# Kernel optimization log

Measured on AMD Instinct MI355X. Metric: run time of the kernel, lower is better.

## Reference

```python
import jax, jax.numpy as jnp
import numpy as np

WS = 8        # window_size
OWIN = 12     # overlap_win_size = int(8*0.5)+8
PAD = 2       # (OWIN - WS)//2
HEADS = 4
DH = 16
INNER = HEADS * DH  # 64
DIM = 64


def _unfold(x, ws=WS, owin=OWIN, pad=PAD):
    # torch nn.Unfold(kernel=(owin,owin), stride=ws, padding=pad):
    # output [b, C*owin*owin, L] with channel ordering (c, kh, kw), L row-major over windows
    b, c, h, w = x.shape
    xp = jnp.pad(x, ((0, 0), (0, 0), (pad, pad), (pad, pad)))
    nH, nW = h // ws, w // ws
    ri = (jnp.arange(nH) * ws)[:, None] + jnp.arange(owin)[None, :]  # [nH, owin]
    ci = (jnp.arange(nW) * ws)[:, None] + jnp.arange(owin)[None, :]  # [nW, owin]
    p = xp[:, :, ri, :]          # [b, c, nH, owin, Wp]
    p = p[:, :, :, :, ci]        # [b, c, nH, owin, nW, owin]
    p = p.transpose(0, 1, 3, 5, 2, 4)  # [b, c, kh, kw, nH, nW]
    return p.reshape(b, c * owin * owin, nH * nW)


def setup_inputs() -> dict:
    key = jax.random.key(0)
    k1, k2, k3 = jax.random.split(key, 3)
    x = jax.random.normal(k1, (1, DIM, 64, 64), jnp.float32)
    w_qkv = jax.random.normal(k2, (3 * INNER, DIM), jnp.float32) * 0.05  # 1x1 conv, no bias
    w_out = jax.random.normal(k3, (DIM, INNER), jnp.float32) * 0.05     # 1x1 conv, no bias
    ln_w = jnp.ones((DIM,), jnp.float32)
    return {"x": x, "w_qkv": w_qkv, "w_out": w_out, "ln_w": ln_w}


def reference(x, w_qkv, w_out, ln_w):
    b, c, h, w = x.shape
    # BiasFree LayerNorm over channel dim (no mean subtraction)
    xc = x.transpose(0, 2, 3, 1)                       # b h w c
    var = jnp.var(xc, axis=-1, keepdims=True)
    xn = (xc / jnp.sqrt(var + 1e-5) * ln_w).transpose(0, 3, 1, 2)
    # qkv 1x1 conv
    qkv = jnp.einsum('bchw,oc->bohw', xn, w_qkv)
    qs, ks, vs = jnp.split(qkv, 3, axis=1)
    # queries: all h*w positions
    qs = qs.transpose(0, 2, 3, 1).reshape(b, h * w, HEADS, DH).transpose(0, 2, 1, 3)  # b heads N dh
    # keys/values: overlapping unfolded windows (faithful to torch reshape order)
    kk = _unfold(ks).reshape(b, INNER, -1).reshape(b, HEADS, -1, DH)  # b heads M dh
    vv = _unfold(vs).reshape(b, INNER, -1).reshape(b, HEADS, -1, DH)
    # rel_pos and fixed_mask are all-zero tensors in the source -> no-op bias
    attn = jnp.einsum('bhnd,bhmd->bhnm', qs, kk) * (DH ** -0.5)
    attn = jax.nn.softmax(attn, axis=-1)
    out = jnp.einsum('bhnm,bhmd->bhnd', attn, vv)
    out = out.transpose(0, 2, 1, 3).reshape(b, h, w, INNER).transpose(0, 3, 1, 2)
    return jnp.einsum('bchw,oc->bohw', out, w_out)
```

## Files before the change

### kernel.cpp

```cpp
#include <hip/hip_runtime.h>
#include <math.h>

#define PIX 4096
typedef unsigned short ushort_t;
typedef unsigned int uint_t;
typedef __attribute__((ext_vector_type(8))) short bf16x8;
typedef __attribute__((ext_vector_type(16))) float f32x16;

#define OFF_APART 524288
#define OFF_USHORT 2752512
#define U_QH 0
#define U_KF 262144
#define U_VF 851968

#define QSCALE 0.36067376022224087f

#if defined(__has_builtin)
#if __has_builtin(__builtin_amdgcn_exp2f)
#define EXP2F(x) __builtin_amdgcn_exp2f(x)
#endif
#if __has_builtin(__builtin_amdgcn_perm)
#define PKHI16(u1, u0) __builtin_amdgcn_perm((u1), (u0), 0x07060302u)
#endif
#endif
#ifndef EXP2F
#define EXP2F(x) exp2f(x)
#endif
#ifndef PKHI16
#define PKHI16(u1, u0) (((u0) >> 16) | ((u1) & 0xFFFF0000u))
#endif

__device__ __forceinline__ ushort_t rn_bf16(float x) {
    uint_t u = __float_as_uint(x);
    return (ushort_t)((u + 0x7FFFu + ((u >> 16) & 1u)) >> 16);
}

__device__ __forceinline__ void split8(const float* v, bf16x8& H, bf16x8& L) {
    union { uint_t u[4]; bf16x8 b; } hh, ll;
    #pragma unroll
    for (int j = 0; j < 4; ++j) {
        uint_t u0 = __float_as_uint(v[2 * j]), u1 = __float_as_uint(v[2 * j + 1]);
        hh.u[j] = PKHI16(u1, u0);
        float l0 = v[2 * j]     - __uint_as_float(u0 & 0xFFFF0000u);
        float l1 = v[2 * j + 1] - __uint_as_float(u1 & 0xFFFF0000u);
        ll.u[j] = PKHI16(__float_as_uint(l1), __float_as_uint(l0));
    }
    H = hh.b; L = ll.b;
}

__global__ __launch_bounds__(256)
void k_nq(const float* __restrict__ x, const float* __restrict__ w_qkv,
          const float* __restrict__ ln_w, float* __restrict__ qkvB,
          ushort_t* __restrict__ QH)
{
    __shared__ float xs[64 * 32];
    __shared__ float red[2][8][32];
    __shared__ float rstd_s[32];
    __shared__ float lw[64];
    __shared__ ushort_t xh[32 * 64];
    __shared__ ushort_t xl[32 * 64];

    const int tid = threadIdx.x;
    const int px = tid & 31, cg = tid >> 5;
    const int pbase = ((int)blockIdx.x >> 1) * 32;
    const int ohalf = blockIdx.x & 1;

    if (tid < 64) lw[tid] = ln_w[tid];
    float s = 0.f, s2 = 0.f;
    #pragma unroll
    for (int cl = 0; cl < 8; ++cl) {
        int c = cg * 8 + cl;
        float v = x[c * PIX + pbase + px];
        xs[c * 32 + px] = v;
        s += v; s2 = fmaf(v, v, s2);
    }
    red[0][cg][px] = s; red[1][cg][px] = s2;
    __syncthreads();
    if (tid < 32) {
        float a = 0.f, b = 0.f;
        #pragma unroll
        for (int gidx = 0; gidx < 8; ++gidx) { a += red[0][gidx][tid]; b += red[1][gidx][tid]; }
        float mean = a * 0.015625f;
        float var  = fmaf(-mean, mean, b * 0.015625f);
        rstd_s[tid] = 1.0f / sqrtf(var + 1e-5f);
    }
    __syncthreads();
    {
        float vals[8];
        const float r = rstd_s[px];
        #pragma unroll
        for (int cl = 0; cl < 8; ++cl) {
            int c = cg * 8 + cl;
            vals[cl] = xs[c * 32 + px] * r * lw[c];
        }
        bf16x8 H, L; split8(vals, H, L);
        const int g = cg ^ (px & 7);
        *(bf16x8*)&xh[px * 64 + g * 8] = H;
        *(bf16x8*)&xl[px * 64 + g * 8] = L;
    }
    __syncthreads();

    const int w = tid >> 6;
    if (w >= 3) return;
    const int l = tid & 63, col = l & 31, rl = l >> 5;
    const int obase = ohalf * 96 + w * 32;

    bf16x8 wh[4], wl[4], xhf[4], xlf[4];
    const float* wrow = w_qkv + (obase + col) * 64;
    #pragma unroll
    for (int s4 = 0; s4 < 4; ++s4) {
        float tmp[8];
        *(float4*)&tmp[0] = *(const float4*)&wrow[s4 * 16 + rl * 8];
        *(float4*)&tmp[4] = *(const float4*)&wrow[s4 * 16 + rl * 8 + 4];
        split8(tmp, wh[s4], wl[s4]);
        const int g = (s4 * 2 + rl) ^ (col & 7);
        xhf[s4] = *(const bf16x8*)&xh[col * 64 + g * 8];
        xlf[s4] = *(const bf16x8*)&xl[col * 64 + g * 8];
    }
    f32x16 acc = {0,0,0,0,0,0,0,0,0,0,0,0,0,0,0,0};
    #pragma unroll
    for (int s4 = 0; s4 < 4; ++s4) {
        acc = __builtin_amdgcn_mfma_f32_32x32x16_bf16(wh[s4], xhf[s4], acc, 0, 0, 0);
        acc = __builtin_amdgcn_mfma_f32_32x32x16_bf16(wl[s4], xhf[s4], acc, 0, 0, 0);
        acc = __builtin_amdgcn_mfma_f32_32x32x16_bf16(wh[s4], xlf[s4], acc, 0, 0, 0);
    }
    const int gpx = pbase + col;
    #pragma unroll
    for (int j = 0; j < 16; ++j) {
        const int o = obase + (j & 3) + 8 * (j >> 2) + 4 * rl;
        if (o < 64) {
            QH[((o >> 4) * PIX + gpx) * 16 + (o & 15)] = rn_bf16(acc[j] * QSCALE);
        } else {
            qkvB[(o - 64) * PIX + gpx] = acc[j];
        }
    }
}

__global__ __launch_bounds__(256)
void k_prep_kv(const float* __restrict__ qkvB,
               ushort_t* __restrict__ KF, ushort_t* __restrict__ VF)
{
    const int bid = blockIdx.x;
    const int tid = threadIdx.x;
    if (bid < 288) {
        const int t = bid * 256 + tid;
        const int h = t / 18432; int r = t - h * 18432;
        const int i = r >> 6;   const int l = r & 63;
        const int col = l & 31, rl = l >> 5;
        const int m = i * 32 + col;
        const int cc = m / 576;  const int r3 = m - cc * 576;
        const int orr = r3 / 48; const int r4 = r3 - orr * 48;
        const int oc = r4 >> 2, wg = r4 & 3;
        const int row = wg * 16 + rl * 8 + orr - 2;
        const bool rowOk = (unsigned)row < 64u;
        const float* src = qkvB + (h * 16 + cc) * PIX + row * 64 + (oc - 2);
        union { ushort_t us[8]; bf16x8 b; } o8;
        #pragma unroll
        for (int j = 0; j < 8; ++j) {
            const int colp = j * 8 + oc - 2;
            const float v = (rowOk && (unsigned)colp < 64u) ? src[j * 8] : 0.f;
            o8.us[j] = rn_bf16(v);
        }
        *(bf16x8*)&KF[(h * 288 + i) * 512 + l * 8] = o8.b;
    } else {
        const int t = (bid - 288) * 256 + tid;
        const int h = t / 18432; int r = t - h * 18432;
        const int i = r >> 6;   const int r2 = r & 63;
        const int half = r2 >> 5; const int rl = (r2 >> 4) & 1; const int colD = r2 & 15;
        const int d = colD;
        const int vcolp = (d & 7) * 8 - 2;
        const int rbase = (d >> 3) * 8 - 2;
        const float* srcp = qkvB + (64 + h * 16) * PIX;
        union { ushort_t us[8]; bf16x8 b; } o8;
        #pragma unroll
        for (int j2 = 0; j2 < 8; ++j2) {
            const int m = i * 32 + half * 16 + rl * 4 + (j2 & 3) + 8 * (j2 >> 2);
            const int cc = m / 576;  const int r3 = m - cc * 576;
            const int orr = r3 / 48; const int r4 = r3 - orr * 48;
            const int oc = r4 >> 2, wg = r4 & 3;
            const int row  = wg * 16 + rbase + orr;
            const int colp = vcolp + oc;
            const bool ok = ((unsigned)row < 64u) && ((unsigned)colp < 64u);
            const float v = ok ? srcp[cc * PIX + row * 64 + colp] : 0.f;
            o8.us[j2] = rn_bf16(v);
        }
        *(bf16x8*)&VF[(h * 288 + i) * 512 + half * 256 + (rl * 16 + colD) * 8] = o8.b;
    }
}

__global__ __launch_bounds__(512)
void k_attn(const ushort_t* __restrict__ QH,
            const ushort_t* __restrict__ KF, const ushort_t* __restrict__ VF,
            float* __restrict__ APart)
{
    const int tid = threadIdx.x;
    const int w   = tid >> 6;
    const int l   = tid & 63;
    const int col = l & 31;
    const int rl  = l >> 5;

    const int bid  = blockIdx.x;
    const int x    = bid & 7;
    const int h    = x >> 1;
    const int tile = ((bid >> 3) << 1) | (x & 1);
    const int qbase = tile * 64;

    const ushort_t* Qb = QH + ((h << 12) + qbase + col) * 16 + rl * 8;
    const bf16x8 qh0 = *(const bf16x8*)&Qb[0];
    const bf16x8 qh1 = *(const bf16x8*)&Qb[512];

    f32x16 acc0 = {0,0,0,0,0,0,0,0,0,0,0,0,0,0,0,0};
    f32x16 acc1 = {0,0,0,0,0,0,0,0,0,0,0,0,0,0,0,0};
    const f32x16 zero = {0,0,0,0,0,0,0,0,0,0,0,0,0,0,0,0};

    union { uint_t u[4]; bf16x8 b; } vconst;
    const uint_t cfill = (col == 16) ? 0x3F803F80u : 0u;
    vconst.u[0] = cfill; vconst.u[1] = cfill; vconst.u[2] = cfill; vconst.u[3] = cfill;

    const ushort_t* kb = KF + (h * 288 + w * 36) * 512;
    const ushort_t* vb = VF + (h * 288 + w * 36) * 512;

    bf16x8 kh = *(const bf16x8*)&kb[l * 8];
    bf16x8 v0 = vconst.b, v1 = vconst.b;
    if (col < 16) {
        v0 = *(const bf16x8*)&vb[(rl * 16 + col) * 8];
        v1 = *(const bf16x8*)&vb[256 + (rl * 16 + col) * 8];
    }

    for (int i = 0; i < 36; ++i) {
        const bf16x8 ckh = kh, cv0 = v0, cv1 = v1;
        if (i < 35) {
            kb += 512; vb += 512;
            kh = *(const bf16x8*)&kb[l * 8];
            if (col < 16) {
                v0 = *(const bf16x8*)&vb[(rl * 16 + col) * 8];
                v1 = *(const bf16x8*)&vb[256 + (rl * 16 + col) * 8];
            }
        }

        f32x16 S0 = __builtin_amdgcn_mfma_f32_32x32x16_bf16(ckh, qh0, zero, 0, 0, 0);
        f32x16 S1 = __builtin_amdgcn_mfma_f32_32x32x16_bf16(ckh, qh1, zero, 0, 0, 0);

        {
            float p[16];
            #pragma unroll
            for (int r = 0; r < 16; ++r) p[r] = EXP2F(S0[r]);
            union { uint_t u[4]; bf16x8 b; } A0, A1;
            #pragma unroll
            for (int j = 0; j < 4; ++j) {
                A0.u[j] = PKHI16(__float_as_uint(p[2 * j + 1]), __float_as_uint(p[2 * j]));
                A1.u[j] = PKHI16(__float_as_uint(p[8 + 2 * j + 1]), __float_as_uint(p[8 + 2 * j]));
            }
            acc0 = __builtin_amdgcn_mfma_f32_32x32x16_bf16(A0.b, cv0, acc0, 0, 0, 0);
            acc0 = __builtin_amdgcn_mfma_f32_32x32x16_bf16(A1.b, cv1, acc0, 0, 0, 0);
        }
        {
            float p[16];
            #pragma unroll
            for (int r = 0; r < 16; ++r) p[r] = EXP2F(S1[r]);
            union { uint_t u[4]; bf16x8 b; } A0, A1;
            #pragma unroll
            for (int j = 0; j < 4; ++j) {
                A0.u[j] = PKHI16(__float_as_uint(p[2 * j + 1]), __float_as_uint(p[2 * j]));
                A1.u[j] = PKHI16(__float_as_uint(p[8 + 2 * j + 1]), __float_as_uint(p[8 + 2 * j]));
            }
            acc1 = __builtin_amdgcn_mfma_f32_32x32x16_bf16(A0.b, cv0, acc1, 0, 0, 0);
            acc1 = __builtin_amdgcn_mfma_f32_32x32x16_bf16(A1.b, cv1, acc1, 0, 0, 0);
        }
    }

    if (col <= 16) {
        float* base = APart + ((size_t)(w * 4 + h) << 12) * 17;
        #pragma unroll
        for (int j = 0; j < 16; ++j) {
            const int q = qbase + (j & 3) + 8 * (j >> 2) + 4 * rl;
            base[q * 17 + col]        = acc0[j];
            base[(q + 32) * 17 + col] = acc1[j];
        }
    }
}

__global__ __launch_bounds__(256)
void k_proj(const float* __restrict__ APart, const float* __restrict__ w_out,
            float* __restrict__ out)
{
    __shared__ float asum[16 * 72];
    __shared__ float wo[64 * 68];
    __shared__ float as2[16 * 68];
    __shared__ float rdn[64];
    const int tid = threadIdx.x;
    const int pbase = blockIdx.x * 16;

    for (int idx = tid; idx < 1088; idx += 256) {
        int q_l = idx / 68; int rem = idx - q_l * 68;
        int h = rem / 17;  int c17 = rem - h * 17;
        float s = 0.f;
        #pragma unroll
        for (int ks = 0; ks < 8; ++ks)
            s += APart[((size_t)((ks * 4 + h) * PIX + pbase + q_l)) * 17 + c17];
        asum[q_l * 72 + h * 17 + c17] = s;
    }
    for (int idx = tid; idx < 4096; idx += 256)
        wo[(idx >> 6) * 68 + (idx & 63)] = w_out[idx];
    __syncthreads();
    if (tid < 64) {
        int h = tid >> 4, px = tid & 15;
        rdn[tid] = 1.0f / asum[px * 72 + h * 17 + 16];
    }
    __syncthreads();
    for (int idx = tid; idx < 1024; idx += 256) {
        int px = idx >> 6, ii = idx & 63;
        int h = ii >> 4, d = ii & 15;
        as2[px * 68 + ii] = asum[px * 72 + h * 17 + d] * rdn[h * 16 + px];
    }
    __syncthreads();

    const int pl = tid & 15;
    const int og = tid >> 4;
    float a0 = 0.f, a1 = 0.f, a2 = 0.f, a3 = 0.f;
    for (int c = 0; c < 64; c += 4) {
        const float4 xv = *(const float4*)&as2[pl * 68 + c];
        const float4 w0 = *(const float4*)&wo[(og * 4 + 0) * 68 + c];
        const float4 w1 = *(const float4*)&wo[(og * 4 + 1) * 68 + c];
        const float4 w2 = *(const float4*)&wo[(og * 4 + 2) * 68 + c];
        const float4 w3 = *(const float4*)&wo[(og * 4 + 3) * 68 + c];
        a0 = fmaf(xv.x, w0.x, fmaf(xv.y, w0.y, fmaf(xv.z, w0.z, fmaf(xv.w, w0.w, a0))));
        a1 = fmaf(xv.x, w1.x, fmaf(xv.y, w1.y, fmaf(xv.z, w1.z, fmaf(xv.w, w1.w, a1))));
        a2 = fmaf(xv.x, w2.x, fmaf(xv.y, w2.y, fmaf(xv.z, w2.z, fmaf(xv.w, w2.w, a2))));
        a3 = fmaf(xv.x, w3.x, fmaf(xv.y, w3.y, fmaf(xv.z, w3.z, fmaf(xv.w, w3.w, a3))));
    }
    out[(og * 4 + 0) * PIX + pbase + pl] = a0;
    out[(og * 4 + 1) * PIX + pbase + pl] = a1;
    out[(og * 4 + 2) * PIX + pbase + pl] = a2;
    out[(og * 4 + 3) * PIX + pbase + pl] = a3;
}

extern "C" void kernel_launch(void* const* d_in, const int* in_sizes, int n_in,
                              void* d_out, int out_size, void* d_ws, size_t ws_size,
                              hipStream_t stream)
{
    const float* x     = (const float*)d_in[0];
    const float* w_qkv = (const float*)d_in[1];
    const float* w_out = (const float*)d_in[2];
    const float* ln_w  = (const float*)d_in[3];
    float* out = (float*)d_out;
    float* ws  = (float*)d_ws;

    float* qkvB  = ws;
    float* APart = ws + OFF_APART;
    ushort_t* U  = (ushort_t*)(ws + OFF_USHORT);
    ushort_t* QH = U + U_QH;
    ushort_t* KF = U + U_KF;
    ushort_t* VF = U + U_VF;

    k_nq      <<<dim3(256), dim3(256), 0, stream>>>(x, w_qkv, ln_w, qkvB, QH);
    k_prep_kv <<<dim3(576), dim3(256), 0, stream>>>(qkvB, KF, VF);
    k_attn    <<<dim3(256), dim3(512), 0, stream>>>(QH, KF, VF, APart);
    k_proj    <<<dim3(256), dim3(256), 0, stream>>>(APart, w_out, out);
}
```

Measured before the change: 96.99 us.

## Simplify QKV projection to single bf16 MFMA and store K/V as bf16

Replaces the split hi/lo bf16 triple-MFMA QKV projection with a single bf16 MFMA per k-step. Each wave now computes its own LayerNorm statistics directly from global memory, with no shared-memory staging or block barriers. K/V intermediates are stored as bf16 instead of fp32, which halves the traffic read by the K/V prep kernel and removes its rounding step. The trade-off is lower projection precision, plus redundant x reads across the six output tiles per pixel tile.

Result: no change. 97.91 us (+1.0%).

```diff
diff --git a/kernel.cpp b/kernel.cpp
--- a/kernel.cpp
+++ b/kernel.cpp
@@ -7,11 +7,11 @@
 typedef __attribute__((ext_vector_type(8))) short bf16x8;
 typedef __attribute__((ext_vector_type(16))) float f32x16;
 
-#define OFF_APART 524288
-#define OFF_USHORT 2752512
+#define OFF_USHORT 2228224
 #define U_QH 0
-#define U_KF 262144
-#define U_VF 851968
+#define U_QKB 262144
+#define U_KF 786432
+#define U_VF 1376256
 
 #define QSCALE 0.36067376022224087f
 
@@ -35,109 +35,73 @@
     return (ushort_t)((u + 0x7FFFu + ((u >> 16) & 1u)) >> 16);
 }
 
-__device__ __forceinline__ void split8(const float* v, bf16x8& H, bf16x8& L) {
-    union { uint_t u[4]; bf16x8 b; } hh, ll;
-    #pragma unroll
-    for (int j = 0; j < 4; ++j) {
-        uint_t u0 = __float_as_uint(v[2 * j]), u1 = __float_as_uint(v[2 * j + 1]);
-        hh.u[j] = PKHI16(u1, u0);
-        float l0 = v[2 * j]     - __uint_as_float(u0 & 0xFFFF0000u);
-        float l1 = v[2 * j + 1] - __uint_as_float(u1 & 0xFFFF0000u);
-        ll.u[j] = PKHI16(__float_as_uint(l1), __float_as_uint(l0));
-    }
-    H = hh.b; L = ll.b;
-}
-
 __global__ __launch_bounds__(256)
-void k_nq(const float* __restrict__ x, const float* __restrict__ w_qkv,
-          const float* __restrict__ ln_w, float* __restrict__ qkvB,
-          ushort_t* __restrict__ QH)
-{
-    __shared__ float xs[64 * 32];
-    __shared__ float red[2][8][32];
-    __shared__ float rstd_s[32];
-    __shared__ float lw[64];
-    __shared__ ushort_t xh[32 * 64];
-    __shared__ ushort_t xl[32 * 64];
-
+void k_qkv(const float* __restrict__ x, const float* __restrict__ w_qkv,
+           const float* __restrict__ ln_w, ushort_t* __restrict__ QH,
+           ushort_t* __restrict__ QKB)
+{
     const int tid = threadIdx.x;
-    const int px = tid & 31, cg = tid >> 5;
-    const int pbase = ((int)blockIdx.x >> 1) * 32;
-    const int ohalf = blockIdx.x & 1;
-
-    if (tid < 64) lw[tid] = ln_w[tid];
+    const int w = tid >> 6, l = tid & 63;
+    const int col = l & 31, half = l >> 5;
+    const int id = (int)blockIdx.x * 4 + w;
+    const int ot = id >> 7;
+    const int pt = id & 127;
+    const int obase = ot * 32;
+    const int gpx = pt * 32 + col;
+
     float s = 0.f, s2 = 0.f;
-    #pragma unroll
-    for (int cl = 0; cl < 8; ++cl) {
-        int c = cg * 8 + cl;
-        float v = x[c * PIX + pbase + px];
-        xs[c * 32 + px] = v;
+    #pragma unroll 16
+    for (int c = 0; c < 64; ++c) {
+        float v = x[c * PIX + gpx];
         s += v; s2 = fmaf(v, v, s2);
     }
-    red[0][cg][px] = s; red[1][cg][px] = s2;
-    __syncthreads();
-    if (tid < 32) {
-        float a = 0.f, b = 0.f;
-        #pragma unroll
-        for (int gidx = 0; gidx < 8; ++gidx) { a += red[0][gidx][tid]; b += red[1][gidx][tid]; }
-        float mean = a * 0.015625f;
-        float var  = fmaf(-mean, mean, b * 0.015625f);
-        rstd_s[tid] = 1.0f / sqrtf(var + 1e-5f);
-    }
-    __syncthreads();
-    {
-        float vals[8];
-        const float r = rstd_s[px];
-        #pragma unroll
-        for (int cl = 0; cl < 8; ++cl) {
-            int c = cg * 8 + cl;
-            vals[cl] = xs[c * 32 + px] * r * lw[c];
-        }
-        bf16x8 H, L; split8(vals, H, L);
-        const int g = cg ^ (px & 7);
-        *(bf16x8*)&xh[px * 64 + g * 8] = H;
-        *(bf16x8*)&xl[px * 64 + g * 8] = L;
-    }
-    __syncthreads();
-
-    const int w = tid >> 6;
-    if (w >= 3) return;
-    const int l = tid & 63, col = l & 31, rl = l >> 5;
-    const int obase = ohalf * 96 + w * 32;
-
-    bf16x8 wh[4], wl[4], xhf[4], xlf[4];
+    const float mean = s * 0.015625f;
+    const float var  = fmaf(-mean, mean, s2 * 0.015625f);
+    const float rs   = 1.0f / sqrtf(var + 1e-5f);
+
+    f32x16 acc = {0,0,0,0,0,0,0,0,0,0,0,0,0,0,0,0};
     const float* wrow = w_qkv + (obase + col) * 64;
     #pragma unroll
     for (int s4 = 0; s4 < 4; ++s4) {
-        float tmp[8];
-        *(float4*)&tmp[0] = *(const float4*)&wrow[s4 * 16 + rl * 8];
-        *(float4*)&tmp[4] = *(const float4*)&wrow[s4 * 16 + rl * 8 + 4];
-        split8(tmp, wh[s4], wl[s4]);
-        const int g = (s4 * 2 + rl) ^ (col & 7);
-        xhf[s4] = *(const bf16x8*)&xh[col * 64 + g * 8];
-        xlf[s4] = *(const bf16x8*)&xl[col * 64 + g * 8];
-    }
-    f32x16 acc = {0,0,0,0,0,0,0,0,0,0,0,0,0,0,0,0};
-    #pragma unroll
-    for (int s4 = 0; s4 < 4; ++s4) {
-        acc = __builtin_amdgcn_mfma_f32_32x32x16_bf16(wh[s4], xhf[s4], acc, 0, 0, 0);
-        acc = __builtin_amdgcn_mfma_f32_32x32x16_bf16(wl[s4], xhf[s4], acc, 0, 0, 0);
-        acc = __builtin_amdgcn_mfma_f32_32x32x16_bf16(wh[s4], xlf[s4], acc, 0, 0, 0);
-    }
-    const int gpx = pbase + col;
+        const int kbase = s4 * 16 + half * 8;
+        float t8[8];
+        *(float4*)&t8[0] = *(const float4*)&wrow[kbase];
+        *(float4*)&t8[4] = *(const float4*)&wrow[kbase + 4];
+        union { uint_t u[4]; bf16x8 b; } wa;
+        #pragma unroll
+        for (int j = 0; j < 4; ++j)
+            wa.u[j] = (uint_t)rn_bf16(t8[2 * j]) | ((uint_t)rn_bf16(t8[2 * j + 1]) << 16);
+        const float4 lwa = *(const float4*)&ln_w[kbase];
+        const float4 lwb = *(const float4*)&ln_w[kbase + 4];
+        float b8[8];
+        b8[0] = x[(kbase + 0) * PIX + gpx] * rs * lwa.x;
+        b8[1] = x[(kbase + 1) * PIX + gpx] * rs * lwa.y;
+        b8[2] = x[(kbase + 2) * PIX + gpx] * rs * lwa.z;
+        b8[3] = x[(kbase + 3) * PIX + gpx] * rs * lwa.w;
+        b8[4] = x[(kbase + 4) * PIX + gpx] * rs * lwb.x;
+        b8[5] = x[(kbase + 5) * PIX + gpx] * rs * lwb.y;
+        b8[6] = x[(kbase + 6) * PIX + gpx] * rs * lwb.z;
+        b8[7] = x[(kbase + 7) * PIX + gpx] * rs * lwb.w;
+        union { uint_t u[4]; bf16x8 b; } xb;
+        #pragma unroll
+        for (int j = 0; j < 4; ++j)
+            xb.u[j] = (uint_t)rn_bf16(b8[2 * j]) | ((uint_t)rn_bf16(b8[2 * j + 1]) << 16);
+        acc = __builtin_amdgcn_mfma_f32_32x32x16_bf16(wa.b, xb.b, acc, 0, 0, 0);
+    }
+
     #pragma unroll
     for (int j = 0; j < 16; ++j) {
-        const int o = obase + (j & 3) + 8 * (j >> 2) + 4 * rl;
+        const int o = obase + (j & 3) + 8 * (j >> 2) + 4 * half;
         if (o < 64) {
             QH[((o >> 4) * PIX + gpx) * 16 + (o & 15)] = rn_bf16(acc[j] * QSCALE);
         } else {
-            qkvB[(o - 64) * PIX + gpx] = acc[j];
+            QKB[(o - 64) * PIX + gpx] = rn_bf16(acc[j]);
         }
     }
 }
 
 __global__ __launch_bounds__(256)
-void k_prep_kv(const float* __restrict__ qkvB,
+void k_prep_kv(const ushort_t* __restrict__ QKB,
                ushort_t* __restrict__ KF, ushort_t* __restrict__ VF)
 {
     const int bid = blockIdx.x;
@@ -153,13 +117,12 @@
         const int oc = r4 >> 2, wg = r4 & 3;
         const int row = wg * 16 + rl * 8 + orr - 2;
         const bool rowOk = (unsigned)row < 64u;
-        const float* src = qkvB + (h * 16 + cc) * PIX + row * 64 + (oc - 2);
+        const ushort_t* src = QKB + (h * 16 + cc) * PIX + row * 64 + (oc - 2);
         union { ushort_t us[8]; bf16x8 b; } o8;
         #pragma unroll
         for (int j = 0; j < 8; ++j) {
             const int colp = j * 8 + oc - 2;
-            const float v = (rowOk && (unsigned)colp < 64u) ? src[j * 8] : 0.f;
-            o8.us[j] = rn_bf16(v);
+            o8.us[j] = (rowOk && (unsigned)colp < 64u) ? src[j * 8] : (ushort_t)0;
         }
         *(bf16x8*)&KF[(h * 288 + i) * 512 + l * 8] = o8.b;
     } else {
@@ -170,7 +133,7 @@
         const int d = colD;
         const int vcolp = (d & 7) * 8 - 2;
         const int rbase = (d >> 3) * 8 - 2;
-        const float* srcp = qkvB + (64 + h * 16) * PIX;
+        const ushort_t* srcp = QKB + (64 + h * 16) * PIX;
         union { ushort_t us[8]; bf16x8 b; } o8;
         #pragma unroll
         for (int j2 = 0; j2 < 8; ++j2) {
@@ -181,8 +144,7 @@
             const int row  = wg * 16 + rbase + orr;
             const int colp = vcolp + oc;
             const bool ok = ((unsigned)row < 64u) && ((unsigned)colp < 64u);
-            const float v = ok ? srcp[cc * PIX + row * 64 + colp] : 0.f;
-            o8.us[j2] = rn_bf16(v);
+            o8.us[j2] = ok ? srcp[cc * PIX + row * 64 + colp] : (ushort_t)0;
         }
         *(bf16x8*)&VF[(h * 288 + i) * 512 + half * 256 + (rl * 16 + colD) * 8] = o8.b;
     }
@@ -346,15 +308,15 @@
     float* out = (float*)d_out;
     float* ws  = (float*)d_ws;
 
-    float* qkvB  = ws;
-    float* APart = ws + OFF_APART;
+    float* APart = ws;
     ushort_t* U  = (ushort_t*)(ws + OFF_USHORT);
-    ushort_t* QH = U + U_QH;
-    ushort_t* KF = U + U_KF;
-    ushort_t* VF = U + U_VF;
-
-    k_nq      <<<dim3(256), dim3(256), 0, stream>>>(x, w_qkv, ln_w, qkvB, QH);
-    k_prep_kv <<<dim3(576), dim3(256), 0, stream>>>(qkvB, KF, VF);
+    ushort_t* QH  = U + U_QH;
+    ushort_t* QKB = U + U_QKB;
+    ushort_t* KF  = U + U_KF;
+    ushort_t* VF  = U + U_VF;
+
+    k_qkv     <<<dim3(192), dim3(256), 0, stream>>>(x, w_qkv, ln_w, QH, QKB);
+    k_prep_kv <<<dim3(576), dim3(256), 0, stream>>>(QKB, KF, VF);
     k_attn    <<<dim3(256), dim3(512), 0, stream>>>(QH, KF, VF, APart);
     k_proj    <<<dim3(256), dim3(256), 0, stream>>>(APart, w_out, out);
 }
```
